# Optimization experiments

Measured on AMD Instinct MI355X. Metric: run time of the kernel, lower is better.

Reference implementation:

```python
import jax, jax.numpy as jnp
import numpy as np

OUT_DIM = 4096
IN_DIM = 4096
N_NNZ = 1600000
BATCH = 8192


def setup_inputs() -> dict:
    key = jax.random.key(0)
    k1, k2, k3 = jax.random.split(key, 3)
    x = jax.random.normal(k1, (BATCH, IN_DIM), dtype=jnp.float32)
    # COO indices of the transposed kernel: (row=output idx, col=input idx)
    rows = jax.random.randint(k2, (N_NNZ, 1), 0, OUT_DIM, dtype=jnp.int64)
    cols = jax.random.randint(jax.random.fold_in(k2, 1), (N_NNZ, 1), 0, IN_DIM, dtype=jnp.int64)
    indices = jnp.concatenate([rows, cols], axis=1)  # (N_NNZ, 2)
    values = jax.random.normal(k3, (N_NNZ,), dtype=jnp.float32) * 0.02
    return {"x": x, "indices": indices, "values": values}


def reference(x, indices, values):
    # kernel_t is a sparse (OUT_DIM, IN_DIM) matrix. In JAX the efficient
    # faithful form is to scatter the nonzeros into a dense matrix (duplicate
    # indices sum, matching SpMM semantics) and do a single dense GEMM.
    rows = indices[:, 0]
    cols = indices[:, 1]
    W_t = jnp.zeros((OUT_DIM, IN_DIM), dtype=values.dtype).at[rows, cols].add(values)
    # output = (kernel_t @ x^T)^T = x @ kernel_t^T, then ReLU activation.
    out = jax.nn.relu(jnp.einsum("bi,oi->bo", x, W_t))
    return out
```

## Files before the change

### kernel.cpp

```cpp
#include <hip/hip_runtime.h>
#include <hip/hip_bf16.h>
#include <stdint.h>

#define M_DIM 8192
#define N_DIM 4096
#define K_DIM 4096
#define NNZ   1600000

typedef __attribute__((ext_vector_type(8))) short bf16x8;
typedef __attribute__((ext_vector_type(4))) float f32x4;

static const size_t WF32_OFF  = 0;
static const size_t WBF16_OFF = 64ull << 20;
static const size_t XB_OFF    = 96ull << 20;
static const size_t WS_NEED   = 160ull << 20;

__device__ __forceinline__ unsigned short f2bf(float f) {
    union { float f; uint32_t u; } a; a.f = f;
    uint32_t u = a.u;
    uint32_t r = (u + 0x7FFFu + ((u >> 16) & 1u)) >> 16;
    return (unsigned short)r;
}

__global__ void scatter_kernel(const int* __restrict__ idx,
                               const float* __restrict__ vals,
                               float* __restrict__ W) {
    int t = blockIdx.x * blockDim.x + threadIdx.x;
    if (t < NNZ) {
        int2 rc = ((const int2*)idx)[t];
        atomicAdd(&W[(size_t)rc.x * K_DIM + rc.y], vals[t]);
    }
}

__global__ void f32_to_bf16_kernel(const float* __restrict__ src,
                                   unsigned short* __restrict__ dst, int n4) {
    int t = blockIdx.x * blockDim.x + threadIdx.x;
    if (t < n4) {
        float4 v = ((const float4*)src)[t];
        ushort4 o;
        o.x = f2bf(v.x); o.y = f2bf(v.y); o.z = f2bf(v.z); o.w = f2bf(v.w);
        ((ushort4*)dst)[t] = o;
    }
}

#define GLOAD16(gp, lp) __builtin_amdgcn_global_load_lds( \
    (const __attribute__((address_space(1))) void*)(gp),  \
    (__attribute__((address_space(3))) void*)(lp), 16, 0, 0)
#define VMCNT(n)   asm volatile("s_waitcnt vmcnt(" #n ")" ::: "memory")
#define BAR()    __builtin_amdgcn_s_barrier()

#define FRAG(T, r, kk) \
    (*(const bf16x8*)&(T)[(r) * 64 + (((((kk) << 2) + l4) ^ ((r) & 7)) << 3)])

#define STAGE_AG(buf, tt, g) \
    GLOAD16(Ab + (size_t)((g) * 64 + rbase) * K_DIM + (size_t)(tt) * 64 + cs, \
            &sA[buf][(g) * 4096 + wid * 512])
#define STAGE_BG(buf, tt, g) \
    GLOAD16(Bb + (size_t)((g) * 64 + rbase) * K_DIM + (size_t)(tt) * 64 + cs, \
            &sB[buf][(g) * 4096 + wid * 512])

__global__ __launch_bounds__(512, 2) void gemm256_v5(
        const __hip_bfloat16* __restrict__ A,
        const __hip_bfloat16* __restrict__ B,
        float* __restrict__ C)
{
    __shared__ __align__(16) __hip_bfloat16 sA[2][256 * 64];
    __shared__ __align__(16) __hip_bfloat16 sB[2][256 * 64];

    const int tid  = threadIdx.x;
    const int lane = tid & 63;
    const int wid  = tid >> 6;
    const int wr   = wid >> 2;
    const int wc   = wid & 3;
    const int l15  = lane & 15, l4 = lane >> 4;

    const int bid = blockIdx.x;
    const int swz = (bid & 7) * 64 + (bid >> 3);
    const int m0  = (swz >> 4) * 256;
    const int n0  = (swz & 15) * 256;

    const int rbase = tid >> 3;
    const int cs    = ((tid & 7) ^ (rbase & 7)) << 3;

    const __hip_bfloat16* Ab = A + (size_t)m0 * K_DIM;
    const __hip_bfloat16* Bb = B + (size_t)n0 * K_DIM;

    f32x4 acc[8][4] = {};

    STAGE_AG(0, 0, 0); STAGE_AG(0, 0, 1); STAGE_AG(0, 0, 2); STAGE_AG(0, 0, 3);
    STAGE_BG(0, 0, 0); STAGE_BG(0, 0, 1); STAGE_BG(0, 0, 2); STAGE_BG(0, 0, 3);
    STAGE_AG(1, 1, 0); STAGE_AG(1, 1, 1); STAGE_AG(1, 1, 2); STAGE_AG(1, 1, 3);
    STAGE_BG(1, 1, 0); STAGE_BG(1, 1, 1);
    VMCNT(6);
    BAR();

    const int NT = K_DIM / 64;
    #pragma unroll 2
    for (int t = 0; t < NT; ++t) {
        const int c = t & 1;
        const __hip_bfloat16* TA = sA[c];
        const __hip_bfloat16* TB = sB[c];

        bf16x8 aLo[4][2], aHi[4][2], bLo[2][2], bHi[2][2];

        #pragma unroll
        for (int m = 0; m < 4; ++m) {
            const int r = wr * 128 + m * 16 + l15;
            aLo[m][0] = FRAG(TA, r, 0);
            aLo[m][1] = FRAG(TA, r, 1);
        }
        #pragma unroll
        for (int n = 0; n < 2; ++n) {
            const int r = wc * 64 + n * 16 + l15;
            bLo[n][0] = FRAG(TB, r, 0);
            bLo[n][1] = FRAG(TB, r, 1);
        }
        BAR();
        __builtin_amdgcn_s_setprio(1);
        #pragma unroll
        for (int k = 0; k < 2; ++k)
            #pragma unroll
            for (int m = 0; m < 4; ++m)
                #pragma unroll
                for (int n = 0; n < 2; ++n)
                    acc[m][n] = __builtin_amdgcn_mfma_f32_16x16x32_bf16(
                                    aLo[m][k], bLo[n][k], acc[m][n], 0, 0, 0);
        __builtin_amdgcn_s_setprio(0);
        if (t + 1 < NT) { STAGE_BG(c ^ 1, t + 1, 2); STAGE_BG(c ^ 1, t + 1, 3); }

        #pragma unroll
        for (int m = 0; m < 4; ++m) {
            const int r = wr * 128 + 64 + m * 16 + l15;
            aHi[m][0] = FRAG(TA, r, 0);
            aHi[m][1] = FRAG(TA, r, 1);
        }
        BAR();
        __builtin_amdgcn_s_setprio(1);
        #pragma unroll
        for (int k = 0; k < 2; ++k)
            #pragma unroll
            for (int m = 0; m < 4; ++m)
                #pragma unroll
                for (int n = 0; n < 2; ++n)
                    acc[4 + m][n] = __builtin_amdgcn_mfma_f32_16x16x32_bf16(
                                    aHi[m][k], bLo[n][k], acc[4 + m][n], 0, 0, 0);
        __builtin_amdgcn_s_setprio(0);

        #pragma unroll
        for (int n = 0; n < 2; ++n) {
            const int r = wc * 64 + 32 + n * 16 + l15;
            bHi[n][0] = FRAG(TB, r, 0);
            bHi[n][1] = FRAG(TB, r, 1);
        }
        BAR();
        __builtin_amdgcn_s_setprio(1);
        #pragma unroll
        for (int k = 0; k < 2; ++k)
            #pragma unroll
            for (int m = 0; m < 4; ++m)
                #pragma unroll
                for (int n = 0; n < 2; ++n)
                    acc[4 + m][2 + n] = __builtin_amdgcn_mfma_f32_16x16x32_bf16(
                                    aHi[m][k], bHi[n][k], acc[4 + m][2 + n], 0, 0, 0);
        __builtin_amdgcn_s_setprio(0);
        if (t + 2 < NT) {
            STAGE_AG(c, t + 2, 0); STAGE_AG(c, t + 2, 1);
            STAGE_AG(c, t + 2, 2); STAGE_AG(c, t + 2, 3);
        }

        BAR();
        __builtin_amdgcn_s_setprio(1);
        #pragma unroll
        for (int k = 0; k < 2; ++k)
            #pragma unroll
            for (int m = 0; m < 4; ++m)
                #pragma unroll
                for (int n = 0; n < 2; ++n)
                    acc[m][2 + n] = __builtin_amdgcn_mfma_f32_16x16x32_bf16(
                                    aLo[m][k], bHi[n][k], acc[m][2 + n], 0, 0, 0);
        __builtin_amdgcn_s_setprio(0);
        if (t + 2 < NT) { STAGE_BG(c, t + 2, 0); STAGE_BG(c, t + 2, 1); }

        if (t < NT - 2) {
            VMCNT(6);
            BAR();
        } else if (t == NT - 2) {
            VMCNT(0);
            BAR();
        }
    }

    const int row_base = m0 + wr * 128;
    const int col_base = n0 + wc * 64;
    #pragma unroll
    for (int m = 0; m < 8; ++m)
        #pragma unroll
        for (int n = 0; n < 4; ++n) {
            const f32x4 v = acc[m][n];
            const int col = col_base + n * 16 + l15;
            #pragma unroll
            for (int j = 0; j < 4; ++j) {
                const int row = row_base + m * 16 + l4 * 4 + j;
                C[(size_t)row * N_DIM + col] = fmaxf(v[j], 0.0f);
            }
        }
}

__global__ void gemm_f32_fallback(const float* __restrict__ A,
                                  const float* __restrict__ W,
                                  float* __restrict__ C) {
    __shared__ float As[64][17];
    __shared__ float Bs[64][17];
    const int tx = threadIdx.x & 15, ty = threadIdx.x >> 4;
    const int m0 = blockIdx.y * 64, n0 = blockIdx.x * 64;
    float acc[4][4] = {};
    for (int kt = 0; kt < K_DIM; kt += 16) {
        #pragma unroll
        for (int i = 0; i < 4; ++i) {
            int e = threadIdx.x + i * 256;
            int r = e >> 4, k = e & 15;
            As[r][k] = A[(size_t)(m0 + r) * K_DIM + kt + k];
            Bs[r][k] = W[(size_t)(n0 + r) * K_DIM + kt + k];
        }
        __syncthreads();
        #pragma unroll
        for (int k = 0; k < 16; ++k) {
            float av[4], bv[4];
            #pragma unroll
            for (int i = 0; i < 4; ++i) av[i] = As[ty * 4 + i][k];
            #pragma unroll
            for (int i = 0; i < 4; ++i) bv[i] = Bs[tx * 4 + i][k];
            #pragma unroll
            for (int i = 0; i < 4; ++i)
                #pragma unroll
                for (int j = 0; j < 4; ++j) acc[i][j] += av[i] * bv[j];
        }
        __syncthreads();
    }
    #pragma unroll
    for (int i = 0; i < 4; ++i)
        #pragma unroll
        for (int j = 0; j < 4; ++j)
            C[(size_t)(m0 + ty * 4 + i) * N_DIM + n0 + tx * 4 + j] =
                fmaxf(acc[i][j], 0.0f);
}

extern "C" void kernel_launch(void* const* d_in, const int* in_sizes, int n_in,
                              void* d_out, int out_size, void* d_ws, size_t ws_size,
                              hipStream_t stream) {
    const float* x       = (const float*)d_in[0];
    const int*   indices = (const int*)d_in[1];
    const float* values  = (const float*)d_in[2];
    float*       out     = (float*)d_out;

    float* Wf = (float*)((char*)d_ws + WF32_OFF);

    hipMemsetAsync(Wf, 0, (size_t)N_DIM * K_DIM * sizeof(float), stream);
    scatter_kernel<<<(NNZ + 255) / 256, 256, 0, stream>>>(indices, values, Wf);

    if (ws_size >= WS_NEED) {
        unsigned short* Wb = (unsigned short*)((char*)d_ws + WBF16_OFF);
        unsigned short* xb = (unsigned short*)((char*)d_ws + XB_OFF);

        {
            int n4 = (N_DIM * K_DIM) / 4;
            f32_to_bf16_kernel<<<(n4 + 255) / 256, 256, 0, stream>>>(Wf, Wb, n4);
        }
        {
            int n4 = (M_DIM * K_DIM) / 4;
            f32_to_bf16_kernel<<<(n4 + 255) / 256, 256, 0, stream>>>(x, xb, n4);
        }

        gemm256_v5<<<(M_DIM / 256) * (N_DIM / 256), 512, 0, stream>>>(
            (const __hip_bfloat16*)xb, (const __hip_bfloat16*)Wb, out);
    } else {
        gemm_f32_fallback<<<dim3(N_DIM / 64, M_DIM / 64), 256, 0, stream>>>(
            x, Wf, out);
    }
}
```

Measured before the change: 362.3 us.

## Fuse W zeroing with x conversion and reorder GEMM inner-loop phases

A single prep kernel now zeroes the fp32 W buffer and converts x to bf16, replacing a separate memset and a conversion launch. In the GEMM main loop, all B fragments (lo and hi) are loaded up front. The MFMA phases are reordered so each 64-wide K step needs three barriers instead of four, and the next-tile B/A global-to-LDS loads are issued at earlier points. This is meant to cut launch and sync overhead and overlap loads better, at the cost of higher register pressure from holding bHi earlier.

```diff
diff --git a/kernel.cpp b/kernel.cpp
--- a/kernel.cpp
+++ b/kernel.cpp
@@ -29,6 +29,23 @@
     if (t < NNZ) {
         int2 rc = ((const int2*)idx)[t];
         atomicAdd(&W[(size_t)rc.x * K_DIM + rc.y], vals[t]);
+    }
+}
+
+__global__ void prep_kernel(float* __restrict__ Wf,
+                            const float* __restrict__ x,
+                            unsigned short* __restrict__ xb,
+                            int nWq, int nTot) {
+    int t = blockIdx.x * blockDim.x + threadIdx.x;
+    if (t >= nTot) return;
+    if (t < nWq) {
+        ((float4*)Wf)[t] = make_float4(0.f, 0.f, 0.f, 0.f);
+    } else {
+        int i = t - nWq;
+        float4 v = ((const float4*)x)[i];
+        ushort4 o;
+        o.x = f2bf(v.x); o.y = f2bf(v.y); o.z = f2bf(v.z); o.w = f2bf(v.w);
+        ((ushort4*)xb)[i] = o;
     }
 }
 
@@ -59,7 +76,7 @@
     GLOAD16(Bb + (size_t)((g) * 64 + rbase) * K_DIM + (size_t)(tt) * 64 + cs, \
             &sB[buf][(g) * 4096 + wid * 512])
 
-__global__ __launch_bounds__(512, 2) void gemm256_v5(
+__global__ __launch_bounds__(512, 2) void gemm256_v9(
         const __hip_bfloat16* __restrict__ A,
         const __hip_bfloat16* __restrict__ B,
         float* __restrict__ C)
@@ -89,8 +106,8 @@
 
     STAGE_AG(0, 0, 0); STAGE_AG(0, 0, 1); STAGE_AG(0, 0, 2); STAGE_AG(0, 0, 3);
     STAGE_BG(0, 0, 0); STAGE_BG(0, 0, 1); STAGE_BG(0, 0, 2); STAGE_BG(0, 0, 3);
+    STAGE_BG(1, 1, 0); STAGE_BG(1, 1, 1);
     STAGE_AG(1, 1, 0); STAGE_AG(1, 1, 1); STAGE_AG(1, 1, 2); STAGE_AG(1, 1, 3);
-    STAGE_BG(1, 1, 0); STAGE_BG(1, 1, 1);
     VMCNT(6);
     BAR();
 
@@ -104,18 +121,19 @@
         bf16x8 aLo[4][2], aHi[4][2], bLo[2][2], bHi[2][2];
 
         #pragma unroll
-        for (int m = 0; m < 4; ++m) {
-            const int r = wr * 128 + m * 16 + l15;
-            aLo[m][0] = FRAG(TA, r, 0);
-            aLo[m][1] = FRAG(TA, r, 1);
-        }
+        for (int n = 0; n < 2; ++n) bLo[n][0] = FRAG(TB, wc * 64 + n * 16 + l15, 0);
+        #pragma unroll
+        for (int m = 0; m < 4; ++m) aLo[m][0] = FRAG(TA, wr * 128 + m * 16 + l15, 0);
+        #pragma unroll
+        for (int n = 0; n < 2; ++n) bLo[n][1] = FRAG(TB, wc * 64 + n * 16 + l15, 1);
+        #pragma unroll
+        for (int m = 0; m < 4; ++m) aLo[m][1] = FRAG(TA, wr * 128 + m * 16 + l15, 1);
         #pragma unroll
         for (int n = 0; n < 2; ++n) {
-            const int r = wc * 64 + n * 16 + l15;
-            bLo[n][0] = FRAG(TB, r, 0);
-            bLo[n][1] = FRAG(TB, r, 1);
-        }
-        BAR();
+            const int r = wc * 64 + 32 + n * 16 + l15;
+            bHi[n][0] = FRAG(TB, r, 0);
+            bHi[n][1] = FRAG(TB, r, 1);
+        }
         __builtin_amdgcn_s_setprio(1);
         #pragma unroll
         for (int k = 0; k < 2; ++k)
@@ -127,15 +145,40 @@
                                     aLo[m][k], bLo[n][k], acc[m][n], 0, 0, 0);
         __builtin_amdgcn_s_setprio(0);
         if (t + 1 < NT) { STAGE_BG(c ^ 1, t + 1, 2); STAGE_BG(c ^ 1, t + 1, 3); }
-
+        BAR();
+
+        if (t + 2 < NT) { STAGE_BG(c, t + 2, 0); STAGE_BG(c, t + 2, 1); }
         #pragma unroll
         for (int m = 0; m < 4; ++m) {
             const int r = wr * 128 + 64 + m * 16 + l15;
             aHi[m][0] = FRAG(TA, r, 0);
             aHi[m][1] = FRAG(TA, r, 1);
         }
+        __builtin_amdgcn_s_setprio(1);
+        #pragma unroll
+        for (int k = 0; k < 2; ++k)
+            #pragma unroll
+            for (int m = 0; m < 4; ++m)
+                #pragma unroll
+                for (int n = 0; n < 2; ++n)
+                    acc[m][2 + n] = __builtin_amdgcn_mfma_f32_16x16x32_bf16(
+                                    aLo[m][k], bHi[n][k], acc[m][2 + n], 0, 0, 0);
+        __builtin_amdgcn_s_setprio(0);
         BAR();
+
+        if (t + 2 < NT) {
+            STAGE_AG(c, t + 2, 0); STAGE_AG(c, t + 2, 1);
+            STAGE_AG(c, t + 2, 2); STAGE_AG(c, t + 2, 3);
+        }
         __builtin_amdgcn_s_setprio(1);
+        #pragma unroll
+        for (int k = 0; k < 2; ++k)
+            #pragma unroll
+            for (int m = 0; m < 4; ++m)
+                #pragma unroll
+                for (int n = 0; n < 2; ++n)
+                    acc[4 + m][2 + n] = __builtin_amdgcn_mfma_f32_16x16x32_bf16(
+                                    aHi[m][k], bHi[n][k], acc[4 + m][2 + n], 0, 0, 0);
         #pragma unroll
         for (int k = 0; k < 2; ++k)
             #pragma unroll
@@ -145,41 +188,6 @@
                     acc[4 + m][n] = __builtin_amdgcn_mfma_f32_16x16x32_bf16(
                                     aHi[m][k], bLo[n][k], acc[4 + m][n], 0, 0, 0);
         __builtin_amdgcn_s_setprio(0);
-
-        #pragma unroll
-        for (int n = 0; n < 2; ++n) {
-            const int r = wc * 64 + 32 + n * 16 + l15;
-            bHi[n][0] = FRAG(TB, r, 0);
-            bHi[n][1] = FRAG(TB, r, 1);
-        }
-        BAR();
-        __builtin_amdgcn_s_setprio(1);
-        #pragma unroll
-        for (int k = 0; k < 2; ++k)
-            #pragma unroll
-            for (int m = 0; m < 4; ++m)
-                #pragma unroll
-                for (int n = 0; n < 2; ++n)
-                    acc[4 + m][2 + n] = __builtin_amdgcn_mfma_f32_16x16x32_bf16(
-                                    aHi[m][k], bHi[n][k], acc[4 + m][2 + n], 0, 0, 0);
-        __builtin_amdgcn_s_setprio(0);
-        if (t + 2 < NT) {
-            STAGE_AG(c, t + 2, 0); STAGE_AG(c, t + 2, 1);
-            STAGE_AG(c, t + 2, 2); STAGE_AG(c, t + 2, 3);
-        }
-
-        BAR();
-        __builtin_amdgcn_s_setprio(1);
-        #pragma unroll
-        for (int k = 0; k < 2; ++k)
-            #pragma unroll
-            for (int m = 0; m < 4; ++m)
-                #pragma unroll
-                for (int n = 0; n < 2; ++n)
-                    acc[m][2 + n] = __builtin_amdgcn_mfma_f32_16x16x32_bf16(
-                                    aLo[m][k], bHi[n][k], acc[m][2 + n], 0, 0, 0);
-        __builtin_amdgcn_s_setprio(0);
-        if (t + 2 < NT) { STAGE_BG(c, t + 2, 0); STAGE_BG(c, t + 2, 1); }
 
         if (t < NT - 2) {
             VMCNT(6);
@@ -255,25 +263,23 @@
 
     float* Wf = (float*)((char*)d_ws + WF32_OFF);
 
-    hipMemsetAsync(Wf, 0, (size_t)N_DIM * K_DIM * sizeof(float), stream);
-    scatter_kernel<<<(NNZ + 255) / 256, 256, 0, stream>>>(indices, values, Wf);
-
     if (ws_size >= WS_NEED) {
         unsigned short* Wb = (unsigned short*)((char*)d_ws + WBF16_OFF);
         unsigned short* xb = (unsigned short*)((char*)d_ws + XB_OFF);
 
-        {
-            int n4 = (N_DIM * K_DIM) / 4;
-            f32_to_bf16_kernel<<<(n4 + 255) / 256, 256, 0, stream>>>(Wf, Wb, n4);
-        }
-        {
-            int n4 = (M_DIM * K_DIM) / 4;
-            f32_to_bf16_kernel<<<(n4 + 255) / 256, 256, 0, stream>>>(x, xb, n4);
-        }
-
-        gemm256_v5<<<(M_DIM / 256) * (N_DIM / 256), 512, 0, stream>>>(
+        const int nWq  = (N_DIM * K_DIM) / 4;
+        const int nTot = nWq + (M_DIM * K_DIM) / 4;
+        prep_kernel<<<(nTot + 255) / 256, 256, 0, stream>>>(Wf, x, xb, nWq, nTot);
+
+        scatter_kernel<<<(NNZ + 255) / 256, 256, 0, stream>>>(indices, values, Wf);
+
+        f32_to_bf16_kernel<<<(nWq + 255) / 256, 256, 0, stream>>>(Wf, Wb, nWq);
+
+        gemm256_v9<<<(M_DIM / 256) * (N_DIM / 256), 512, 0, stream>>>(
             (const __hip_bfloat16*)xb, (const __hip_bfloat16*)Wb, out);
     } else {
+        hipMemsetAsync(Wf, 0, (size_t)N_DIM * K_DIM * sizeof(float), stream);
+        scatter_kernel<<<(NNZ + 255) / 256, 256, 0, stream>>>(indices, values, Wf);
         gemm_f32_fallback<<<dim3(N_DIM / 64, M_DIM / 64), 256, 0, stream>>>(
             x, Wf, out);
     }
```

New measurement: 383.1 us. 5.7% more time.
